# Kernel tuning notes

Measured on AMD Instinct MI355X. Metric: run time of the kernel, lower is better.

The kernel has to match this reference:

```python
import jax, jax.numpy as jnp
import numpy as np
from jax import lax

T, B, INPUT, HID, OUT, FUT = 128, 1024, 4, 512, 4, 32


def setup_inputs() -> dict:
    key = jax.random.key(0)
    ks = jax.random.split(key, 12)
    s = 0.05  # small init like uniform(-1/sqrt(H), 1/sqrt(H))
    inp = {
        "x": jax.random.normal(ks[0], (T, B, INPUT), jnp.float32),
        "Wih1": jax.random.normal(ks[1], (4 * HID, INPUT), jnp.float32) * s,
        "Whh1": jax.random.normal(ks[2], (4 * HID, HID), jnp.float32) * s,
        "bih1": jax.random.normal(ks[3], (4 * HID,), jnp.float32) * s,
        "bhh1": jax.random.normal(ks[4], (4 * HID,), jnp.float32) * s,
        "Wih2": jax.random.normal(ks[5], (4 * HID, HID), jnp.float32) * s,
        "Whh2": jax.random.normal(ks[6], (4 * HID, HID), jnp.float32) * s,
        "bih2": jax.random.normal(ks[7], (4 * HID,), jnp.float32) * s,
        "bhh2": jax.random.normal(ks[8], (4 * HID,), jnp.float32) * s,
        "Wl": jax.random.normal(ks[9], (OUT, HID), jnp.float32) * s,
        "bl": jax.random.normal(ks[10], (OUT,), jnp.float32) * s,
        "future": FUT,
    }
    return inp


def _cell(xt, h, c, Wih, Whh, bih, bhh):
    # PyTorch LSTMCell gate order: i, f, g, o
    g = xt @ Wih.T + bih + h @ Whh.T + bhh  # [B, 4H]
    i, f, gg, o = jnp.split(g, 4, axis=-1)
    c = jax.nn.sigmoid(f) * c + jax.nn.sigmoid(i) * jnp.tanh(gg)
    h = jax.nn.sigmoid(o) * jnp.tanh(c)
    return h, c


def reference(x, Wih1, Whh1, bih1, bhh1, Wih2, Whh2, bih2, bhh2, Wl, bl, future):
    nb = x.shape[1]
    H = Whh1.shape[1]
    z = jnp.zeros((nb, H), x.dtype)

    def step1(carry, xt):
        h1, c1, h2, c2 = carry
        h1, c1 = _cell(xt, h1, c1, Wih1, Whh1, bih1, bhh1)
        h2, c2 = _cell(h1, h2, c2, Wih2, Whh2, bih2, bhh2)
        return (h1, c1, h2, c2), None

    (h1, c1, h2, c2), _ = lax.scan(step1, (z, z, z, z), x)
    tmp_out = h2  # frozen last hidden of cell 2 (faithful to original bug)

    def step2(carry, _):
        h1, c1, h2, c2 = carry
        # original future loop reuses lstm2 weights for both updates
        h1, c1 = _cell(tmp_out, h1, c1, Wih2, Whh2, bih2, bhh2)
        h2, c2 = _cell(h1, h2, c2, Wih2, Whh2, bih2, bhh2)
        out = h2 @ Wl.T + bl  # [B, OUT]
        return (h1, c1, h2, c2), out

    _, outs = lax.scan(step2, (h1, c1, h2, c2), None, length=future)
    return outs  # [future, B, OUT]
```

## Files before the change

kernel.cpp:

```cpp
#include <hip/hip_runtime.h>

typedef _Float16 v8h __attribute__((ext_vector_type(8)));
typedef float v4f __attribute__((ext_vector_type(4)));
typedef unsigned int uint;

#define OFF_BAR   0
#define OFF_AO0   4096
#define OFF_AO1   (OFF_AO0 + (1<<21))
#define OFF_AF0   (OFF_AO1 + (1<<21))
#define OFF_AF1   (OFF_AF0 + (1<<21))
#define OFF_W1    (OFF_AF1 + (1<<21))
#define OFF_W2    (OFF_W1 + (1<<21))
#define OFF_B1    (OFF_W2 + (1<<22))
#define OFF_B2    (OFF_B1 + 8192)

__global__ __launch_bounds__(256, 1)
void lstm_prep(const float* __restrict__ Whh1, const float* __restrict__ Wih2,
               const float* __restrict__ Whh2, const float* __restrict__ bih1,
               const float* __restrict__ bhh1, const float* __restrict__ bih2,
               const float* __restrict__ bhh2,
               _Float16* __restrict__ W1p, _Float16* __restrict__ W2p,
               float* __restrict__ bs1, float* __restrict__ bs2)
{
  const int total = 1048576 + 2097152 + 4096;
  for (int i = blockIdx.x*blockDim.x + threadIdx.x; i < total; i += gridDim.x*blockDim.x) {
    if (i < 1048576) {
      int nt = i >> 13, rem = i & 8191;
      int k32 = rem >> 9, c = rem & 511;
      int lane = c >> 3, el = c & 7;
      int n = nt*16 + (lane & 15);
      int k = k32*32 + (lane >> 4)*8 + el;
      W1p[i] = (_Float16)Whh1[n*512 + k];
    } else if (i < 3145728) {
      int j = i - 1048576;
      int nt = j >> 14, rem = j & 16383;
      int k32 = rem >> 9, c = rem & 511;
      int lane = c >> 3, el = c & 7;
      int n = nt*16 + (lane & 15);
      int k = k32*32 + (lane >> 4)*8 + el;
      float v = (k < 512) ? Wih2[n*512 + k] : Whh2[n*512 + (k - 512)];
      W2p[j] = (_Float16)v;
    } else {
      int n = i - 3145728;
      if (n < 2048) bs1[n] = bih1[n] + bhh1[n];
      else          bs2[n-2048] = bih2[n-2048] + bhh2[n-2048];
    }
  }
}

__device__ __forceinline__ float sigmoidf_(float z) { return 1.f / (1.f + __expf(-z)); }
__device__ __forceinline__ float tanhf_(float z)    { return 1.f - 2.f/(1.f + __expf(2.f*z)); }

__device__ __forceinline__ v8h ld_frag_dev(const _Float16* base, uint off) {
  union { unsigned long long u[2]; v8h h; } cv;
  const unsigned long long* q = (const unsigned long long*)(base + off);
  cv.u[0] = __hip_atomic_load(q,     __ATOMIC_RELAXED, __HIP_MEMORY_SCOPE_AGENT);
  cv.u[1] = __hip_atomic_load(q + 1, __ATOMIC_RELAXED, __HIP_MEMORY_SCOPE_AGENT);
  return cv.h;
}

__global__ __launch_bounds__(512, 2)
void lstm_main(const float* __restrict__ x, const float* __restrict__ Wih1,
               const float* __restrict__ Wl, const float* __restrict__ blv,
               _Float16* __restrict__ AO0, _Float16* __restrict__ AO1,
               _Float16* __restrict__ AF0, _Float16* __restrict__ AF1,
               const _Float16* __restrict__ W1, const _Float16* __restrict__ W2,
               const float* __restrict__ bs1, const float* __restrict__ bs2,
               int* __restrict__ bar, float* __restrict__ out)
{
  __shared__ float lred[16384];
  const int tid  = threadIdx.x;
  const int wv   = tid >> 6, lane = tid & 63;
  const int quad = lane >> 4, lc = lane & 15;
  const int cw   = wv & 1;
  const int mtb  = (wv >> 1) & 1;
  const int kh   = wv >> 2;
  const int bid  = blockIdx.x;
  const int jg   = bid >> 3;
  const int ht   = (bid & 7)*2 + (jg >> 4);
  const int bt   = jg & 15;

  _Float16* const AOv[2] = {AO0, AO1};
  _Float16* const AFv[2] = {AF0, AF1};

  const int erow = tid >> 3, enib = tid & 7;
  const int tid2  = tid - 256;
  const int b_loc = (tid2 >= 0) ? (tid2 >> 2) : 0, oct = tid2 & 3;
  const int m     = b_loc & 15, mtile_e = bt*4 + (b_loc >> 4);
  const int STASH = 8448;

  int ntg_[8];
  #pragma unroll
  for (int tt = 0; tt < 8; tt++) ntg_[tt] = (tt>>1)*32 + ht*2 + (tt&1);

  float c1s[4], c2s[4];
  #pragma unroll
  for (int i = 0; i < 4; i++) { c1s[i] = 0.f; c2s[i] = 0.f; }

  for (int r = 0; r < 162; r++) {
    const bool p1 = r < 129;
    const int  f  = r - 129;
    const int  wp = p1 ? (r & 1) : (f & 1);
    const int  rp = wp ^ 1;
    const _Float16* A1 = p1 ? AOv[rp] : AFv[rp];
    const _Float16* A2 = AOv[rp];
    const bool skip1 = (r == 128 || r == 161);
    const bool skip2 = (r == 0   || r == 129);

    const _Float16* Ac = cw ? A2 : A1;
    const _Float16* Bc = cw ? W2 : (p1 ? W1 : W2);
    const int wk   = cw ? 32 : (p1 ? 16 : 32);
    const int half = cw ? 16 : (p1 ? 8 : 16);
    const int ch0  = kh * half;

    v4f acc[2][8];
    #pragma unroll
    for (int i2 = 0; i2 < 2; i2++)
      #pragma unroll
      for (int tt = 0; tt < 8; tt++) acc[i2][tt] = (v4f){0,0,0,0};

    uint aoff[2];
    #pragma unroll
    for (int i2 = 0; i2 < 2; i2++)
      aoff[i2] = (uint)(((bt*4 + mtb*2 + i2)*32 + ch0)*512 + lane*8);
    uint boff[8];
    #pragma unroll
    for (int tt = 0; tt < 8; tt++)
      boff[tt] = (uint)((ntg_[tt]*wk + ch0)*512 + lane*8);

    #pragma unroll 4
    for (int cc = 0; cc < half; cc++) {
      v8h av[2];
      #pragma unroll
      for (int i2 = 0; i2 < 2; i2++)
        av[i2] = ld_frag_dev(Ac, aoff[i2] + cc*512);
      #pragma unroll
      for (int tt = 0; tt < 8; tt++) {
        v8h bv = *(const v8h*)(Bc + boff[tt] + cc*512);
        #pragma unroll
        for (int i2 = 0; i2 < 2; i2++)
          acc[i2][tt] = __builtin_amdgcn_mfma_f32_16x16x32_f16(av[i2], bv, acc[i2][tt], 0, 0, 0);
      }
    }

    const int rbase = (cw*2 + mtb) * 4096;
    if (kh) {
      #pragma unroll
      for (int i2 = 0; i2 < 2; i2++)
        #pragma unroll
        for (int tt = 0; tt < 8; tt++)
          *(v4f*)&lred[rbase + ((i2*8 + tt)*64 + lane)*4] = acc[i2][tt];
    }
    __syncthreads();
    if (!kh) {
      #pragma unroll
      for (int i2 = 0; i2 < 2; i2++)
        #pragma unroll
        for (int tt = 0; tt < 8; tt++)
          acc[i2][tt] += *(const v4f*)&lred[rbase + ((i2*8 + tt)*64 + lane)*4];
    }
    __syncthreads();

    if (!kh && cw == 0) {
      #pragma unroll
      for (int i2 = 0; i2 < 2; i2++)
        #pragma unroll
        for (int tt = 0; tt < 8; tt++) {
          int row = (mtb*2 + i2)*16 + quad*4;
          int col = tt*16 + lc;
          #pragma unroll
          for (int rr = 0; rr < 4; rr++) lred[(row + rr)*132 + col] = acc[i2][tt][rr];
        }
    }
    __syncthreads();

    {
      const float* bsx = p1 ? bs1 : bs2;
      float g[4][4];
      #pragma unroll
      for (int g4 = 0; g4 < 4; g4++) {
        v4f gv = *(const v4f*)&lred[erow*132 + g4*32 + enib*4];
        v4f bv = *(const v4f*)&bsx[g4*512 + ht*32 + enib*4];
        #pragma unroll
        for (int j = 0; j < 4; j++) g[g4][j] = gv[j] + bv[j];
      }
      if (p1 && r < 128) {
        const v4f xv = *(const v4f*)(x + ((size_t)r*1024 + bt*64 + erow)*4);
        #pragma unroll
        for (int g4 = 0; g4 < 4; g4++)
          #pragma unroll
          for (int j = 0; j < 4; j++) {
            int hh = ht*32 + enib*4 + j;
            const v4f w = *(const v4f*)(Wih1 + (size_t)(g4*512 + hh)*4);
            g[g4][j] += xv[0]*w[0] + xv[1]*w[1] + xv[2]*w[2] + xv[3]*w[3];
          }
      }
      if (!skip1) {
        v4f hf;
        #pragma unroll
        for (int j = 0; j < 4; j++) {
          float ig = sigmoidf_(g[0][j]), fg = sigmoidf_(g[1][j]);
          float gg = tanhf_(g[2][j]),    og = sigmoidf_(g[3][j]);
          float c = fg*c1s[j] + ig*gg;
          c1s[j] = c;
          hf[j] = og * tanhf_(c);
        }
        *(v4f*)&lred[STASH + erow*36 + enib*4] = hf;
      }
    }
    __syncthreads();

    if (tid >= 256 && !skip1) {
      v4f h0 = *(const v4f*)&lred[STASH + b_loc*36 + oct*8];
      v4f h1 = *(const v4f*)&lred[STASH + b_loc*36 + oct*8 + 4];
      union { _Float16 h8[8]; unsigned long long u[2]; } hu;
      #pragma unroll
      for (int j = 0; j < 4; j++) { hu.h8[j] = (_Float16)h0[j]; hu.h8[4+j] = (_Float16)h1[j]; }
      auto st16 = [&](_Float16* bp, int chunk) {
        unsigned long long* p = (unsigned long long*)
          (bp + (((size_t)(mtile_e*32 + chunk)) << 9) + (oct*16 + m)*8);
        __hip_atomic_store(p,     hu.u[0], __ATOMIC_RELAXED, __HIP_MEMORY_SCOPE_AGENT);
        __hip_atomic_store(p + 1, hu.u[1], __ATOMIC_RELAXED, __HIP_MEMORY_SCOPE_AGENT);
      };
      if (p1) {
        st16(AOv[wp], ht);
        if (r == 127) st16(AFv[1], 16 + ht);
      } else {
        st16(AFv[wp], 16 + ht);
        st16(AOv[wp], ht);
      }
    }
    if (!kh && cw == 1) {
      #pragma unroll
      for (int i2 = 0; i2 < 2; i2++)
        #pragma unroll
        for (int tt = 0; tt < 8; tt++) {
          int row = (mtb*2 + i2)*16 + quad*4;
          int col = tt*16 + lc;
          #pragma unroll
          for (int rr = 0; rr < 4; rr++) lred[(row + rr)*132 + col] = acc[i2][tt][rr];
        }
    }
    __syncthreads();

    {
      float g[4][4];
      #pragma unroll
      for (int g4 = 0; g4 < 4; g4++) {
        v4f gv = *(const v4f*)&lred[erow*132 + g4*32 + enib*4];
        v4f bv = *(const v4f*)&bs2[g4*512 + ht*32 + enib*4];
        #pragma unroll
        for (int j = 0; j < 4; j++) g[g4][j] = gv[j] + bv[j];
      }
      if (!skip2) {
        v4f hf;
        #pragma unroll
        for (int j = 0; j < 4; j++) {
          float ig = sigmoidf_(g[0][j]), fg = sigmoidf_(g[1][j]);
          float gg = tanhf_(g[2][j]),    og = sigmoidf_(g[3][j]);
          float c = fg*c2s[j] + ig*gg;
          c2s[j] = c;
          hf[j] = og * tanhf_(c);
        }
        *(v4f*)&lred[STASH + erow*36 + enib*4] = hf;
      }
    }
    __syncthreads();

    if (tid >= 256 && !skip2) {
      v4f h0 = *(const v4f*)&lred[STASH + b_loc*36 + oct*8];
      v4f h1 = *(const v4f*)&lred[STASH + b_loc*36 + oct*8 + 4];
      union { _Float16 h8[8]; unsigned long long u[2]; } hu;
      #pragma unroll
      for (int j = 0; j < 4; j++) { hu.h8[j] = (_Float16)h0[j]; hu.h8[4+j] = (_Float16)h1[j]; }
      auto st16 = [&](_Float16* bp, int chunk) {
        unsigned long long* p = (unsigned long long*)
          (bp + (((size_t)(mtile_e*32 + chunk)) << 9) + (oct*16 + m)*8);
        __hip_atomic_store(p,     hu.u[0], __ATOMIC_RELAXED, __HIP_MEMORY_SCOPE_AGENT);
        __hip_atomic_store(p + 1, hu.u[1], __ATOMIC_RELAXED, __HIP_MEMORY_SCOPE_AGENT);
      };
      st16(AOv[wp], 16 + ht);
      if (r == 128) { st16(AFv[0], ht); st16(AFv[1], ht); }
    }
    if (tid < 256 && !p1 && r >= 130) {
      const int s = r - 130;
      int bb = tid >> 2, o = tid & 3;
      float sa = (ht == 0) ? blv[o] : 0.f;
      const float* wl = Wl + (size_t)o*512 + ht*32;
      #pragma unroll
      for (int jj = 0; jj < 32; jj++) sa += lred[STASH + bb*36 + jj] * wl[jj];
      atomicAdd(&out[(((size_t)s*1024) + bt*64 + bb)*4 + o], sa);
    }
    __syncthreads();

    if (tid == 0) {
      int* ctr = bar + bt*32;
      __hip_atomic_fetch_add(ctr, 1, __ATOMIC_RELAXED, __HIP_MEMORY_SCOPE_AGENT);
      const int target = 16*(r+1);
      while (__hip_atomic_load(ctr, __ATOMIC_RELAXED, __HIP_MEMORY_SCOPE_AGENT) < target)
        __builtin_amdgcn_s_sleep(1);
    }
    __syncthreads();
  }
}

extern "C" void kernel_launch(void* const* d_in, const int* in_sizes, int n_in,
                              void* d_out, int out_size, void* d_ws, size_t ws_size,
                              hipStream_t stream) {
  const float* x    = (const float*)d_in[0];
  const float* Wih1 = (const float*)d_in[1];
  const float* Whh1 = (const float*)d_in[2];
  const float* bih1 = (const float*)d_in[3];
  const float* bhh1 = (const float*)d_in[4];
  const float* Wih2 = (const float*)d_in[5];
  const float* Whh2 = (const float*)d_in[6];
  const float* bih2 = (const float*)d_in[7];
  const float* bhh2 = (const float*)d_in[8];
  const float* Wl   = (const float*)d_in[9];
  const float* bl   = (const float*)d_in[10];

  char* ws = (char*)d_ws;
  int*      bar = (int*)(ws + OFF_BAR);
  _Float16* AO0 = (_Float16*)(ws + OFF_AO0);
  _Float16* AO1 = (_Float16*)(ws + OFF_AO1);
  _Float16* AF0 = (_Float16*)(ws + OFF_AF0);
  _Float16* AF1 = (_Float16*)(ws + OFF_AF1);
  _Float16* W1p = (_Float16*)(ws + OFF_W1);
  _Float16* W2p = (_Float16*)(ws + OFF_W2);
  float*    bs1 = (float*)(ws + OFF_B1);
  float*    bs2 = (float*)(ws + OFF_B2);

  hipMemsetAsync(ws, 0, (size_t)OFF_W1, stream);
  hipMemsetAsync(d_out, 0, (size_t)out_size * sizeof(float), stream);

  lstm_prep<<<2048, 256, 0, stream>>>(Whh1, Wih2, Whh2, bih1, bhh1, bih2, bhh2,
                                      W1p, W2p, bs1, bs2);
  lstm_main<<<256, 512, 0, stream>>>(x, Wih1, Wl, bl, AO0, AO1, AF0, AF1,
                                     W1p, W2p, bs1, bs2, bar, (float*)d_out);
}
```

Measured before the change: 3.106 ms.

## Fuse LSTM gate epilogue into MFMA accumulator registers, cut syncthreads

The LSTM cell nonlinearities now run directly on the MFMA accumulators in the waves that hold the reduced results, instead of scattering gates to LDS and re-reading them in a separate elementwise pass. Both cells' epilogues run concurrently across the waves. The wave-to-cell mapping is swizzled so the K-split reduction pairs line up, and biases and Wih1 columns are preloaded into registers. This removes several block barriers and LDS round trips per step, at the cost of more registers and only half the waves doing the epilogue.

```diff
diff --git a/kernel.cpp b/kernel.cpp
--- a/kernel.cpp
+++ b/kernel.cpp
@@ -50,6 +50,7 @@
 
 __device__ __forceinline__ float sigmoidf_(float z) { return 1.f / (1.f + __expf(-z)); }
 __device__ __forceinline__ float tanhf_(float z)    { return 1.f - 2.f/(1.f + __expf(2.f*z)); }
+__device__ __forceinline__ float dot4_(v4f a, v4f b){ return a[0]*b[0]+a[1]*b[1]+a[2]*b[2]+a[3]*b[3]; }
 
 __device__ __forceinline__ v8h ld_frag_dev(const _Float16* base, uint off) {
   union { unsigned long long u[2]; v8h h; } cv;
@@ -72,9 +73,9 @@
   const int tid  = threadIdx.x;
   const int wv   = tid >> 6, lane = tid & 63;
   const int quad = lane >> 4, lc = lane & 15;
-  const int cw   = wv & 1;
+  const int kh   = wv >> 2;
+  const int cw   = (wv & 1) ^ kh;
   const int mtb  = (wv >> 1) & 1;
-  const int kh   = wv >> 2;
   const int bid  = blockIdx.x;
   const int jg   = bid >> 3;
   const int ht   = (bid & 7)*2 + (jg >> 4);
@@ -83,19 +84,33 @@
   _Float16* const AOv[2] = {AO0, AO1};
   _Float16* const AFv[2] = {AF0, AF1};
 
-  const int erow = tid >> 3, enib = tid & 7;
   const int tid2  = tid - 256;
   const int b_loc = (tid2 >= 0) ? (tid2 >> 2) : 0, oct = tid2 & 3;
   const int m     = b_loc & 15, mtile_e = bt*4 + (b_loc >> 4);
-  const int STASH = 8448;
 
   int ntg_[8];
   #pragma unroll
   for (int tt = 0; tt < 8; tt++) ntg_[tt] = (tt>>1)*32 + ht*2 + (tt&1);
 
-  float c1s[4], c2s[4];
+  float b1r[8], b2r[8];
+  v4f   w1r[4][2];
+  if (!kh) {
+    #pragma unroll
+    for (int g = 0; g < 4; g++)
+      #pragma unroll
+      for (int u = 0; u < 2; u++) {
+        const int col = g*512 + ht*32 + u*16 + lc;
+        b1r[g*2+u] = bs1[col];
+        b2r[g*2+u] = bs2[col];
+        w1r[g][u]  = *(const v4f*)(Wih1 + (size_t)col*4);
+      }
+  }
+
+  float cst[16];
   #pragma unroll
-  for (int i = 0; i < 4; i++) { c1s[i] = 0.f; c2s[i] = 0.f; }
+  for (int i = 0; i < 16; i++) cst[i] = 0.f;
+
+  const int rbase = (cw*2 + mtb) * 4096;
 
   for (int r = 0; r < 162; r++) {
     const bool p1 = r < 129;
@@ -143,7 +158,6 @@
       }
     }
 
-    const int rbase = (cw*2 + mtb) * 4096;
     if (kh) {
       #pragma unroll
       for (int i2 = 0; i2 < 2; i2++)
@@ -152,143 +166,92 @@
           *(v4f*)&lred[rbase + ((i2*8 + tt)*64 + lane)*4] = acc[i2][tt];
     }
     __syncthreads();
+
     if (!kh) {
+      const bool xterm = (cw == 0) && p1 && (r < 128);
+      v4f xr[2][4];
+      if (xterm) {
+        #pragma unroll
+        for (int i2 = 0; i2 < 2; i2++)
+          #pragma unroll
+          for (int rr = 0; rr < 4; rr++)
+            xr[i2][rr] = *(const v4f*)(x + ((size_t)r*1024 + bt*64
+                              + (mtb*2 + i2)*16 + quad*4 + rr)*4);
+      }
       #pragma unroll
       for (int i2 = 0; i2 < 2; i2++)
         #pragma unroll
         for (int tt = 0; tt < 8; tt++)
           acc[i2][tt] += *(const v4f*)&lred[rbase + ((i2*8 + tt)*64 + lane)*4];
+
+      const bool skipc = cw ? skip2 : skip1;
+      if (!skipc) {
+        const bool useb1 = (cw == 0) && p1;
+        #pragma unroll
+        for (int i2 = 0; i2 < 2; i2++)
+          #pragma unroll
+          for (int u = 0; u < 2; u++)
+            #pragma unroll
+            for (int rr = 0; rr < 4; rr++) {
+              float gi = acc[i2][0+u][rr] + (useb1 ? b1r[0+u] : b2r[0+u]);
+              float gf = acc[i2][2+u][rr] + (useb1 ? b1r[2+u] : b2r[2+u]);
+              float gg = acc[i2][4+u][rr] + (useb1 ? b1r[4+u] : b2r[4+u]);
+              float go = acc[i2][6+u][rr] + (useb1 ? b1r[6+u] : b2r[6+u]);
+              if (xterm) {
+                gi += dot4_(xr[i2][rr], w1r[0][u]);
+                gf += dot4_(xr[i2][rr], w1r[1][u]);
+                gg += dot4_(xr[i2][rr], w1r[2][u]);
+                go += dot4_(xr[i2][rr], w1r[3][u]);
+              }
+              const float ig = sigmoidf_(gi), fg = sigmoidf_(gf);
+              const float g2 = tanhf_(gg),    og = sigmoidf_(go);
+              const int ci = (i2*2 + u)*4 + rr;
+              const float c = fg*cst[ci] + ig*g2;
+              cst[ci] = c;
+              lred[rbase + (i2*16 + quad*4 + rr)*36 + u*16 + lc] = og * tanhf_(c);
+            }
+      }
     }
     __syncthreads();
 
-    if (!kh && cw == 0) {
-      #pragma unroll
-      for (int i2 = 0; i2 < 2; i2++)
-        #pragma unroll
-        for (int tt = 0; tt < 8; tt++) {
-          int row = (mtb*2 + i2)*16 + quad*4;
-          int col = tt*16 + lc;
-          #pragma unroll
-          for (int rr = 0; rr < 4; rr++) lred[(row + rr)*132 + col] = acc[i2][tt][rr];
-        }
-    }
-    __syncthreads();
-
-    {
-      const float* bsx = p1 ? bs1 : bs2;
-      float g[4][4];
-      #pragma unroll
-      for (int g4 = 0; g4 < 4; g4++) {
-        v4f gv = *(const v4f*)&lred[erow*132 + g4*32 + enib*4];
-        v4f bv = *(const v4f*)&bsx[g4*512 + ht*32 + enib*4];
-        #pragma unroll
-        for (int j = 0; j < 4; j++) g[g4][j] = gv[j] + bv[j];
-      }
-      if (p1 && r < 128) {
-        const v4f xv = *(const v4f*)(x + ((size_t)r*1024 + bt*64 + erow)*4);
-        #pragma unroll
-        for (int g4 = 0; g4 < 4; g4++)
-          #pragma unroll
-          for (int j = 0; j < 4; j++) {
-            int hh = ht*32 + enib*4 + j;
-            const v4f w = *(const v4f*)(Wih1 + (size_t)(g4*512 + hh)*4);
-            g[g4][j] += xv[0]*w[0] + xv[1]*w[1] + xv[2]*w[2] + xv[3]*w[3];
-          }
-      }
-      if (!skip1) {
-        v4f hf;
-        #pragma unroll
-        for (int j = 0; j < 4; j++) {
-          float ig = sigmoidf_(g[0][j]), fg = sigmoidf_(g[1][j]);
-          float gg = tanhf_(g[2][j]),    og = sigmoidf_(g[3][j]);
-          float c = fg*c1s[j] + ig*gg;
-          c1s[j] = c;
-          hf[j] = og * tanhf_(c);
-        }
-        *(v4f*)&lred[STASH + erow*36 + enib*4] = hf;
-      }
-    }
-    __syncthreads();
-
-    if (tid >= 256 && !skip1) {
-      v4f h0 = *(const v4f*)&lred[STASH + b_loc*36 + oct*8];
-      v4f h1 = *(const v4f*)&lred[STASH + b_loc*36 + oct*8 + 4];
+    if (tid >= 256) {
       union { _Float16 h8[8]; unsigned long long u[2]; } hu;
-      #pragma unroll
-      for (int j = 0; j < 4; j++) { hu.h8[j] = (_Float16)h0[j]; hu.h8[4+j] = (_Float16)h1[j]; }
       auto st16 = [&](_Float16* bp, int chunk) {
         unsigned long long* p = (unsigned long long*)
           (bp + (((size_t)(mtile_e*32 + chunk)) << 9) + (oct*16 + m)*8);
         __hip_atomic_store(p,     hu.u[0], __ATOMIC_RELAXED, __HIP_MEMORY_SCOPE_AGENT);
         __hip_atomic_store(p + 1, hu.u[1], __ATOMIC_RELAXED, __HIP_MEMORY_SCOPE_AGENT);
       };
-      if (p1) {
-        st16(AOv[wp], ht);
-        if (r == 127) st16(AFv[1], 16 + ht);
-      } else {
-        st16(AFv[wp], 16 + ht);
-        st16(AOv[wp], ht);
-      }
-    }
-    if (!kh && cw == 1) {
-      #pragma unroll
-      for (int i2 = 0; i2 < 2; i2++)
-        #pragma unroll
-        for (int tt = 0; tt < 8; tt++) {
-          int row = (mtb*2 + i2)*16 + quad*4;
-          int col = tt*16 + lc;
-          #pragma unroll
-          for (int rr = 0; rr < 4; rr++) lred[(row + rr)*132 + col] = acc[i2][tt][rr];
+      if (!skip1) {
+        const float* sp = &lred[(b_loc >> 5)*4096 + (b_loc & 31)*36 + oct*8];
+        v4f h0 = *(const v4f*)sp, h1v = *(const v4f*)(sp + 4);
+        #pragma unroll
+        for (int j = 0; j < 4; j++) { hu.h8[j] = (_Float16)h0[j]; hu.h8[4+j] = (_Float16)h1v[j]; }
+        if (p1) {
+          st16(AOv[wp], ht);
+          if (r == 127) st16(AFv[1], 16 + ht);
+        } else {
+          st16(AFv[wp], 16 + ht);
+          st16(AOv[wp], ht);
         }
-    }
-    __syncthreads();
-
-    {
-      float g[4][4];
-      #pragma unroll
-      for (int g4 = 0; g4 < 4; g4++) {
-        v4f gv = *(const v4f*)&lred[erow*132 + g4*32 + enib*4];
-        v4f bv = *(const v4f*)&bs2[g4*512 + ht*32 + enib*4];
-        #pragma unroll
-        for (int j = 0; j < 4; j++) g[g4][j] = gv[j] + bv[j];
       }
       if (!skip2) {
-        v4f hf;
-        #pragma unroll
-        for (int j = 0; j < 4; j++) {
-          float ig = sigmoidf_(g[0][j]), fg = sigmoidf_(g[1][j]);
-          float gg = tanhf_(g[2][j]),    og = sigmoidf_(g[3][j]);
-          float c = fg*c2s[j] + ig*gg;
-          c2s[j] = c;
-          hf[j] = og * tanhf_(c);
-        }
-        *(v4f*)&lred[STASH + erow*36 + enib*4] = hf;
-      }
-    }
-    __syncthreads();
-
-    if (tid >= 256 && !skip2) {
-      v4f h0 = *(const v4f*)&lred[STASH + b_loc*36 + oct*8];
-      v4f h1 = *(const v4f*)&lred[STASH + b_loc*36 + oct*8 + 4];
-      union { _Float16 h8[8]; unsigned long long u[2]; } hu;
-      #pragma unroll
-      for (int j = 0; j < 4; j++) { hu.h8[j] = (_Float16)h0[j]; hu.h8[4+j] = (_Float16)h1[j]; }
-      auto st16 = [&](_Float16* bp, int chunk) {
-        unsigned long long* p = (unsigned long long*)
-          (bp + (((size_t)(mtile_e*32 + chunk)) << 9) + (oct*16 + m)*8);
-        __hip_atomic_store(p,     hu.u[0], __ATOMIC_RELAXED, __HIP_MEMORY_SCOPE_AGENT);
-        __hip_atomic_store(p + 1, hu.u[1], __ATOMIC_RELAXED, __HIP_MEMORY_SCOPE_AGENT);
-      };
-      st16(AOv[wp], 16 + ht);
-      if (r == 128) { st16(AFv[0], ht); st16(AFv[1], ht); }
+        const float* sp = &lred[(2 + (b_loc >> 5))*4096 + (b_loc & 31)*36 + oct*8];
+        v4f h0 = *(const v4f*)sp, h1v = *(const v4f*)(sp + 4);
+        #pragma unroll
+        for (int j = 0; j < 4; j++) { hu.h8[j] = (_Float16)h0[j]; hu.h8[4+j] = (_Float16)h1v[j]; }
+        st16(AOv[wp], 16 + ht);
+        if (r == 128) { st16(AFv[0], ht); st16(AFv[1], ht); }
+      }
     }
     if (tid < 256 && !p1 && r >= 130) {
       const int s = r - 130;
       int bb = tid >> 2, o = tid & 3;
       float sa = (ht == 0) ? blv[o] : 0.f;
       const float* wl = Wl + (size_t)o*512 + ht*32;
-      #pragma unroll
-      for (int jj = 0; jj < 32; jj++) sa += lred[STASH + bb*36 + jj] * wl[jj];
+      const float* sp = &lred[(2 + (bb >> 5))*4096 + (bb & 31)*36];
+      #pragma unroll
+      for (int jj = 0; jj < 32; jj++) sa += sp[jj] * wl[jj];
       atomicAdd(&out[(((size_t)s*1024) + bt*64 + bb)*4 + o], sa);
     }
     __syncthreads();
```

Result: slower. 6.221 ms (+100.3%).
